# Optimization experiments

Measured on AMD Instinct MI355X. Metric: run time of the kernel, lower is better.

Reference implementation:

```python
import jax, jax.numpy as jnp
import numpy as np

H = 64; W = 64          # input resolution
WS = 8                  # window size
SHIFT = 4               # shift size (= WS//2)
C = 384                 # dim
NH = 12                 # num heads
HD = C // NH            # head dim
HID = 4 * C             # mlp hidden
N = WS * WS             # tokens per window
NWIN = (H // WS) * (W // WS)
EPS = 1e-5


def _rel_pos_index():
    coords = np.stack(np.meshgrid(np.arange(WS), np.arange(WS), indexing='ij'))  # [2,WS,WS]
    flat = coords.reshape(2, -1)                                                 # [2,N]
    rel = flat[:, :, None] - flat[:, None, :]                                    # [2,N,N]
    rel = rel.transpose(1, 2, 0).copy()                                          # [N,N,2]
    rel[..., 0] += WS - 1
    rel[..., 1] += WS - 1
    rel[..., 0] *= 2 * WS - 1
    return rel.sum(-1)                                                           # [N,N]


def _attn_mask():
    img = np.zeros((H, W))
    cnt = 0
    for hs in (slice(0, -WS), slice(-WS, -SHIFT), slice(-SHIFT, None)):
        for ws_ in (slice(0, -WS), slice(-WS, -SHIFT), slice(-SHIFT, None)):
            img[hs, ws_] = cnt
            cnt += 1
    mw = img.reshape(H // WS, WS, W // WS, WS).transpose(0, 2, 1, 3).reshape(-1, N)  # [nW,N]
    diff = mw[:, None, :] - mw[:, :, None]                                           # [nW,N,N]
    return np.where(diff != 0, -100.0, 0.0).astype(np.float32)


_REL_IDX = jnp.asarray(_rel_pos_index())
_MASK = jnp.asarray(_attn_mask())


def _ln(x, g, b):
    m = jnp.mean(x, axis=-1, keepdims=True)
    v = jnp.mean((x - m) ** 2, axis=-1, keepdims=True)
    return (x - m) * jax.lax.rsqrt(v + EPS) * g + b


def _win_partition(x):
    # [B,H,W,C] -> [B*nW, N, C]
    B = x.shape[0]
    x = x.reshape(B, H // WS, WS, W // WS, WS, C).transpose(0, 1, 3, 2, 4, 5)
    return x.reshape(-1, N, C)


def _win_reverse(w, B):
    # [B*nW, N, C] -> [B,H,W,C]
    x = w.reshape(B, H // WS, W // WS, WS, WS, C).transpose(0, 1, 3, 2, 4, 5)
    return x.reshape(B, H, W, C)


def setup_inputs() -> dict:
    key = jax.random.key(0)
    ks = jax.random.split(key, 8)
    s = 0.02
    return {
        'x': jax.random.normal(ks[0], (32, H * W, C), jnp.float32),
        'gamma1': jnp.ones((C,), jnp.float32),
        'beta1': jnp.zeros((C,), jnp.float32),
        'w_qkv': jax.random.normal(ks[1], (C, 3 * C), jnp.float32) * s,
        'b_qkv': jnp.zeros((3 * C,), jnp.float32),
        'bias_table': jax.random.normal(ks[2], ((2 * WS - 1) ** 2, NH), jnp.float32) * s,
        'w_proj': jax.random.normal(ks[3], (C, C), jnp.float32) * s,
        'b_proj': jnp.zeros((C,), jnp.float32),
        'gamma2': jnp.ones((C,), jnp.float32),
        'beta2': jnp.zeros((C,), jnp.float32),
        'w_fc1': jax.random.normal(ks[4], (C, HID), jnp.float32) * s,
        'b_fc1': jnp.zeros((HID,), jnp.float32),
        'w_fc2': jax.random.normal(ks[5], (HID, C), jnp.float32) * s,
        'b_fc2': jnp.zeros((C,), jnp.float32),
    }


def reference(x, gamma1, beta1, w_qkv, b_qkv, bias_table, w_proj, b_proj,
              gamma2, beta2, w_fc1, b_fc1, w_fc2, b_fc2):
    B, L, _ = x.shape
    shortcut = x
    h = _ln(x, gamma1, beta1).reshape(B, H, W, C)
    h = jnp.roll(h, shift=(-SHIFT, -SHIFT), axis=(1, 2))
    xw = _win_partition(h)                                     # [B*nW, N, C]
    Bw = xw.shape[0]

    qkv = (xw @ w_qkv + b_qkv).reshape(Bw, N, 3, NH, HD)
    qkv = qkv.transpose(2, 0, 3, 1, 4)                         # [3, Bw, NH, N, HD]
    q, k, v = qkv[0], qkv[1], qkv[2]
    q = q * (HD ** -0.5)
    attn = jnp.einsum('bhnd,bhmd->bhnm', q, k)                 # [Bw, NH, N, N]

    rel_bias = bias_table[_REL_IDX.reshape(-1)].reshape(N, N, NH).transpose(2, 0, 1)
    attn = attn + rel_bias[None]
    attn = attn.reshape(B, NWIN, NH, N, N) + _MASK[None, :, None]
    attn = jax.nn.softmax(attn.reshape(Bw, NH, N, N), axis=-1)

    out = jnp.einsum('bhnm,bhmd->bhnd', attn, v)               # [Bw, NH, N, HD]
    out = out.transpose(0, 2, 1, 3).reshape(Bw, N, C)
    out = out @ w_proj + b_proj

    h = _win_reverse(out, B)
    h = jnp.roll(h, shift=(SHIFT, SHIFT), axis=(1, 2)).reshape(B, L, C)
    x = shortcut + h

    m = _ln(x, gamma2, beta2)
    m = jax.nn.gelu(m @ w_fc1 + b_fc1, approximate=False) @ w_fc2 + b_fc2
    return x + m
```

## Files before the change

### kernel.cpp

```cpp
#include <hip/hip_runtime.h>
#include <hip/hip_bf16.h>

typedef __bf16 bf16_t;
typedef __bf16 bf16x8 __attribute__((ext_vector_type(8)));
typedef float f32x4 __attribute__((ext_vector_type(4)));

#define DI __device__ __forceinline__

static constexpr int TOK = 131072;
static constexpr int NWIN = 2048;

DI int src_token(int t) {
  int b = t >> 12;
  int widx = (t >> 6) & 63;
  int n = t & 63;
  int wh = widx >> 3, ww = widx & 7;
  int i = n >> 3, j = n & 7;
  int y = ((wh << 3) + i + 4) & 63;
  int x2 = ((ww << 3) + j + 4) & 63;
  return (b << 12) + (y << 6) + x2;
}

DI f32x4 mfma16(bf16x8 a, bf16x8 b, f32x4 c) {
  return __builtin_amdgcn_mfma_f32_16x16x32_bf16(a, b, c, 0, 0, 0);
}

DI void gload_lds16(const bf16_t* g, bf16_t* l) {
  __builtin_amdgcn_global_load_lds(
      (__attribute__((address_space(1))) void*)const_cast<bf16_t*>(g),
      (__attribute__((address_space(3))) void*)l, 16, 0, 0);
}

__global__ void wconv_kernel(const float* __restrict__ w, bf16_t* __restrict__ wt,
                             int K, int N) {
  int idx = blockIdx.x * 256 + threadIdx.x;
  if (idx >= N * K) return;
  int n = idx / K, k = idx - n * K;
  wt[idx] = (bf16_t)w[(size_t)k * N + n];
}

template <int MAP>
__global__ __launch_bounds__(256)
void ln_kernel(const float* __restrict__ xin, const float* __restrict__ g,
               const float* __restrict__ be, bf16_t* __restrict__ out) {
  int w = threadIdx.x >> 6, l = threadIdx.x & 63;
  int t = blockIdx.x * 4 + w;
  int s = MAP ? src_token(t) : t;
  const float* row = xin + (size_t)s * 384;
  float v[6], s1 = 0.f, s2 = 0.f;
#pragma unroll
  for (int i = 0; i < 6; i++) {
    v[i] = row[l + i * 64];
    s1 += v[i];
    s2 += v[i] * v[i];
  }
#pragma unroll
  for (int o = 32; o; o >>= 1) {
    s1 += __shfl_xor(s1, o);
    s2 += __shfl_xor(s2, o);
  }
  float mean = s1 * (1.f / 384.f);
  float var = s2 * (1.f / 384.f) - mean * mean;
  float rs = rsqrtf(var + 1e-5f);
  bf16_t* orow = out + (size_t)t * 384;
#pragma unroll
  for (int i = 0; i < 6; i++) {
    int idx = l + i * 64;
    orow[idx] = (bf16_t)((v[i] - mean) * rs * g[idx] + be[idx]);
  }
}

template <int MODE>
__global__ __launch_bounds__(256, 4)
void gemm_bt(const bf16_t* __restrict__ A, const bf16_t* __restrict__ Wt,
             const float* __restrict__ bias, int K, int ldout, int ncols,
             bf16_t* outb, float* outf, const float* resid) {
  __shared__ __align__(16) bf16_t Alds[128 * 64];
  __shared__ __align__(16) bf16_t Blds[128 * 64];
  const int tid = threadIdx.x;
  const int l = tid & 63, w = tid >> 6;
  const int lr = l & 15, lq = l >> 4;
  const int nwg = gridDim.x;
  const int orig = blockIdx.x;
  const int wgid = (orig & 7) * (nwg >> 3) + (orig >> 3);
  const int bn = wgid % ncols, bm = wgid / ncols;
  const int wr = w >> 1, wc = w & 1;
  const size_t rowA0 = (size_t)bm * 128, rowB0 = (size_t)bn * 128;

  f32x4 acc[4][4] = {};
  for (int k0 = 0; k0 < K; k0 += 64) {
#pragma unroll
    for (int r = 0; r < 4; r++) {
      int offb = r * 2048 + w * 512;
      int off = offb + l * 8;
      int row = off >> 6;
      int slot = (off >> 3) & 7;
      int scol = (slot ^ (row & 7)) << 3;
      gload_lds16(A + (rowA0 + row) * K + k0 + scol, &Alds[offb]);
      gload_lds16(Wt + (rowB0 + row) * K + k0 + scol, &Blds[offb]);
    }
    __syncthreads();
#pragma unroll
    for (int ks = 0; ks < 2; ks++) {
      bf16x8 af[4], bfr[4];
#pragma unroll
      for (int fi = 0; fi < 4; fi++) {
        int row = wr * 64 + fi * 16 + lr;
        af[fi] = *(const bf16x8*)&Alds[row * 64 +
                                       ((ks * 32 + lq * 8) ^ ((row & 7) << 3))];
      }
#pragma unroll
      for (int fj = 0; fj < 4; fj++) {
        int row = wc * 64 + fj * 16 + lr;
        bfr[fj] = *(const bf16x8*)&Blds[row * 64 +
                                        ((ks * 32 + lq * 8) ^ ((row & 7) << 3))];
      }
#pragma unroll
      for (int fi = 0; fi < 4; fi++)
#pragma unroll
        for (int fj = 0; fj < 4; fj++)
          acc[fi][fj] = mfma16(af[fi], bfr[fj], acc[fi][fj]);
    }
    __syncthreads();
  }

#pragma unroll
  for (int fi = 0; fi < 4; fi++) {
#pragma unroll
    for (int reg = 0; reg < 4; reg++) {
      int grow = bm * 128 + wr * 64 + fi * 16 + lq * 4 + reg;
      size_t rbase;
      if constexpr (MODE == 2)
        rbase = (size_t)src_token(grow) * ldout;
      else
        rbase = (size_t)grow * ldout;
#pragma unroll
      for (int fj = 0; fj < 4; fj++) {
        int gcol = bn * 128 + wc * 64 + fj * 16 + lr;
        float val = acc[fi][fj][reg] + bias[gcol];
        if constexpr (MODE == 0) {
          outb[rbase + gcol] = (bf16_t)val;
        } else if constexpr (MODE == 1) {
          val = 0.5f * val * (1.f + erff(val * 0.70710678118f));
          outb[rbase + gcol] = (bf16_t)val;
        } else {
          outf[rbase + gcol] = val + resid[rbase + gcol];
        }
      }
    }
  }
}

__global__ __launch_bounds__(64)
void attn_kernel(const bf16_t* __restrict__ qkv, const float* __restrict__ btab,
                 bf16_t* __restrict__ aout) {
  __shared__ __align__(16) bf16_t Qs[64 * 32];
  __shared__ __align__(16) bf16_t Ks[64 * 32];
  __shared__ __align__(16) bf16_t Vt[32 * 64];
  __shared__ __align__(16) bf16_t Ps[64 * 64];
  const int win = blockIdx.x, h = blockIdx.y;
  const int l = threadIdx.x, lr = l & 15, lq = l >> 4;

  {
    const bf16_t* qrow = qkv + ((size_t)win * 64 + l) * 1152 + h * 32;
#pragma unroll
    for (int c = 0; c < 4; c++) {
      *(bf16x8*)&Qs[l * 32 + c * 8] = *(const bf16x8*)&qrow[c * 8];
      *(bf16x8*)&Ks[l * 32 + c * 8] = *(const bf16x8*)&qrow[384 + c * 8];
    }
#pragma unroll
    for (int c = 0; c < 4; c++) {
      bf16x8 tv = *(const bf16x8*)&qrow[768 + c * 8];
#pragma unroll
      for (int e = 0; e < 8; e++) {
        int vr = c * 8 + e;
        Vt[vr * 64 + (l ^ ((vr & 7) << 3))] = tv[e];
      }
    }
  }
  __syncthreads();

  f32x4 sacc[4][4] = {};
  {
    bf16x8 a[4], b[4];
#pragma unroll
    for (int fi = 0; fi < 4; fi++)
      a[fi] = *(const bf16x8*)&Qs[(fi * 16 + lr) * 32 + lq * 8];
#pragma unroll
    for (int fj = 0; fj < 4; fj++)
      b[fj] = *(const bf16x8*)&Ks[(fj * 16 + lr) * 32 + lq * 8];
#pragma unroll
    for (int fi = 0; fi < 4; fi++)
#pragma unroll
      for (int fj = 0; fj < 4; fj++)
        sacc[fi][fj] = mfma16(a[fi], b[fj], sacc[fi][fj]);
  }

  const int widx = win & 63;
  const int wh = widx >> 3, ww = widx & 7;
  const float scale = 0.17677669529663687f;
#pragma unroll
  for (int fi = 0; fi < 4; fi++) {
#pragma unroll
    for (int reg = 0; reg < 4; reg++) {
      int row = fi * 16 + lq * 4 + reg;
      int i1 = row >> 3, j1 = row & 7;
      int ly1 = (wh == 7) ? (i1 >= 4 ? 2 : 1) : 0;
      int lx1 = (ww == 7) ? (j1 >= 4 ? 2 : 1) : 0;
      float vals[4], m = -1e30f;
#pragma unroll
      for (int fj = 0; fj < 4; fj++) {
        int col = fj * 16 + lr;
        int i2 = col >> 3, j2 = col & 7;
        float v = sacc[fi][fj][reg] * scale +
                  btab[((i1 - i2 + 7) * 15 + (j1 - j2 + 7)) * 12 + h];
        int ly2 = (wh == 7) ? (i2 >= 4 ? 2 : 1) : 0;
        int lx2 = (ww == 7) ? (j2 >= 4 ? 2 : 1) : 0;
        if (ly1 != ly2 || lx1 != lx2) v -= 100.f;
        vals[fj] = v;
        m = fmaxf(m, v);
      }
#pragma unroll
      for (int o = 1; o < 16; o <<= 1) m = fmaxf(m, __shfl_xor(m, o));
      float ssum = 0.f;
#pragma unroll
      for (int fj = 0; fj < 4; fj++) {
        vals[fj] = __expf(vals[fj] - m);
        ssum += vals[fj];
      }
#pragma unroll
      for (int o = 1; o < 16; o <<= 1) ssum += __shfl_xor(ssum, o);
      float inv = 1.f / ssum;
      int sw = (row & 7) << 3;
#pragma unroll
      for (int fj = 0; fj < 4; fj++)
        Ps[row * 64 + ((fj * 16 + lr) ^ sw)] = (bf16_t)(vals[fj] * inv);
    }
  }
  __syncthreads();

  f32x4 oacc[4][2] = {};
#pragma unroll
  for (int kc = 0; kc < 2; kc++) {
    bf16x8 pa[4], vb[2];
#pragma unroll
    for (int fi = 0; fi < 4; fi++) {
      int row = fi * 16 + lr;
      pa[fi] = *(const bf16x8*)&Ps[row * 64 + ((kc * 32 + lq * 8) ^ ((row & 7) << 3))];
    }
#pragma unroll
    for (int fj = 0; fj < 2; fj++) {
      int row = fj * 16 + lr;
      vb[fj] = *(const bf16x8*)&Vt[row * 64 + ((kc * 32 + lq * 8) ^ ((row & 7) << 3))];
    }
#pragma unroll
    for (int fi = 0; fi < 4; fi++)
#pragma unroll
      for (int fj = 0; fj < 2; fj++)
        oacc[fi][fj] = mfma16(pa[fi], vb[fj], oacc[fi][fj]);
  }
#pragma unroll
  for (int fi = 0; fi < 4; fi++)
#pragma unroll
    for (int reg = 0; reg < 4; reg++) {
      int row = fi * 16 + lq * 4 + reg;
      size_t rb = ((size_t)win * 64 + row) * 384 + h * 32;
#pragma unroll
      for (int fj = 0; fj < 2; fj++)
        aout[rb + fj * 16 + lr] = (bf16_t)oacc[fi][fj][reg];
    }
}

extern "C" void kernel_launch(void* const* d_in, const int* in_sizes, int n_in,
                              void* d_out, int out_size, void* d_ws, size_t ws_size,
                              hipStream_t stream) {
  (void)in_sizes; (void)n_in; (void)out_size; (void)ws_size;
  const float* x      = (const float*)d_in[0];
  const float* gamma1 = (const float*)d_in[1];
  const float* beta1  = (const float*)d_in[2];
  const float* w_qkv  = (const float*)d_in[3];
  const float* b_qkv  = (const float*)d_in[4];
  const float* btab   = (const float*)d_in[5];
  const float* w_proj = (const float*)d_in[6];
  const float* b_proj = (const float*)d_in[7];
  const float* gamma2 = (const float*)d_in[8];
  const float* beta2  = (const float*)d_in[9];
  const float* w_fc1  = (const float*)d_in[10];
  const float* b_fc1  = (const float*)d_in[11];
  const float* w_fc2  = (const float*)d_in[12];
  const float* b_fc2  = (const float*)d_in[13];
  float* out = (float*)d_out;

  char* ws = (char*)d_ws;
  size_t off = 0;
  auto alloc = [&](size_t bytes) {
    void* p = ws + off;
    off += (bytes + 255) & ~(size_t)255;
    return p;
  };
  bf16_t* wqkvT  = (bf16_t*)alloc((size_t)1152 * 384 * 2);
  bf16_t* wprojT = (bf16_t*)alloc((size_t)384 * 384 * 2);
  bf16_t* wfc1T  = (bf16_t*)alloc((size_t)1536 * 384 * 2);
  bf16_t* wfc2T  = (bf16_t*)alloc((size_t)384 * 1536 * 2);
  char* big = (char*)alloc((size_t)TOK * 1536 * 2);
  bf16_t* bufA = (bf16_t*)big;
  bf16_t* bufH = (bf16_t*)big;
  bf16_t* bufB = (bf16_t*)alloc((size_t)TOK * 384 * 2);

  wconv_kernel<<<(1152 * 384 + 255) / 256, 256, 0, stream>>>(w_qkv, wqkvT, 384, 1152);
  wconv_kernel<<<(384 * 384 + 255) / 256, 256, 0, stream>>>(w_proj, wprojT, 384, 384);
  wconv_kernel<<<(384 * 1536 + 255) / 256, 256, 0, stream>>>(w_fc1, wfc1T, 384, 1536);
  wconv_kernel<<<(1536 * 384 + 255) / 256, 256, 0, stream>>>(w_fc2, wfc2T, 1536, 384);

  ln_kernel<1><<<TOK / 4, 256, 0, stream>>>(x, gamma1, beta1, bufB);
  gemm_bt<0><<<9 * (TOK / 128), 256, 0, stream>>>(
      bufB, wqkvT, b_qkv, 384, 1152, 9, bufA, nullptr, nullptr);
  attn_kernel<<<dim3(NWIN, 12), 64, 0, stream>>>(bufA, btab, bufB);
  gemm_bt<2><<<3 * (TOK / 128), 256, 0, stream>>>(
      bufB, wprojT, b_proj, 384, 384, 3, nullptr, out, x);
  ln_kernel<0><<<TOK / 4, 256, 0, stream>>>(out, gamma2, beta2, bufB);
  gemm_bt<1><<<12 * (TOK / 128), 256, 0, stream>>>(
      bufB, wfc1T, b_fc1, 384, 1536, 12, bufH, nullptr, nullptr);
  gemm_bt<3><<<3 * (TOK / 128), 256, 0, stream>>>(
      bufH, wfc2T, b_fc2, 1536, 384, 3, nullptr, out, out);
}
```

Measured before the change: 1.212 ms.

## Replace LDS-staged GEMM with direct global-to-register fragment loads and double buffering

The GEMM no longer stages A and W tiles through shared memory with global_load_lds and barriers. Each wave now loads its MFMA fragments straight from global memory into registers, double-buffered across K steps of 32, and the occupancy hint drops from 4 to 3 blocks. This removes LDS traffic and __syncthreads, but the two waves sharing a row or column block now each fetch the same data, and the 16-byte loads per lane are strided by K, which may hurt coalescing and cache efficiency.

Result: slower. 2.246 ms (+85.4%).

```diff
diff --git a/kernel.cpp b/kernel.cpp
--- a/kernel.cpp
+++ b/kernel.cpp
@@ -25,12 +25,6 @@
   return __builtin_amdgcn_mfma_f32_16x16x32_bf16(a, b, c, 0, 0, 0);
 }
 
-DI void gload_lds16(const bf16_t* g, bf16_t* l) {
-  __builtin_amdgcn_global_load_lds(
-      (__attribute__((address_space(1))) void*)const_cast<bf16_t*>(g),
-      (__attribute__((address_space(3))) void*)l, 16, 0, 0);
-}
-
 __global__ void wconv_kernel(const float* __restrict__ w, bf16_t* __restrict__ wt,
                              int K, int N) {
   int idx = blockIdx.x * 256 + threadIdx.x;
@@ -71,12 +65,10 @@
 }
 
 template <int MODE>
-__global__ __launch_bounds__(256, 4)
-void gemm_bt(const bf16_t* __restrict__ A, const bf16_t* __restrict__ Wt,
-             const float* __restrict__ bias, int K, int ldout, int ncols,
-             bf16_t* outb, float* outf, const float* resid) {
-  __shared__ __align__(16) bf16_t Alds[128 * 64];
-  __shared__ __align__(16) bf16_t Blds[128 * 64];
+__global__ __launch_bounds__(256, 3)
+void gemm_gather(const bf16_t* __restrict__ A, const bf16_t* __restrict__ Wt,
+                 const float* __restrict__ bias, int K, int ldout, int ncols,
+                 bf16_t* outb, float* outf, const float* resid) {
   const int tid = threadIdx.x;
   const int l = tid & 63, w = tid >> 6;
   const int lr = l & 15, lq = l >> 4;
@@ -85,50 +77,50 @@
   const int wgid = (orig & 7) * (nwg >> 3) + (orig >> 3);
   const int bn = wgid % ncols, bm = wgid / ncols;
   const int wr = w >> 1, wc = w & 1;
-  const size_t rowA0 = (size_t)bm * 128, rowB0 = (size_t)bn * 128;
+  const size_t row0 = (size_t)bm * 128 + wr * 64;
+  const size_t col0 = (size_t)bn * 128 + wc * 64;
+
+  const bf16_t* pa = A + (row0 + lr) * K + lq * 8;
+  const bf16_t* pb = Wt + (col0 + lr) * K + lq * 8;
+  const size_t fstride = (size_t)16 * K;
 
   f32x4 acc[4][4] = {};
-  for (int k0 = 0; k0 < K; k0 += 64) {
-#pragma unroll
-    for (int r = 0; r < 4; r++) {
-      int offb = r * 2048 + w * 512;
-      int off = offb + l * 8;
-      int row = off >> 6;
-      int slot = (off >> 3) & 7;
-      int scol = (slot ^ (row & 7)) << 3;
-      gload_lds16(A + (rowA0 + row) * K + k0 + scol, &Alds[offb]);
-      gload_lds16(Wt + (rowB0 + row) * K + k0 + scol, &Blds[offb]);
-    }
-    __syncthreads();
-#pragma unroll
-    for (int ks = 0; ks < 2; ks++) {
-      bf16x8 af[4], bfr[4];
-#pragma unroll
-      for (int fi = 0; fi < 4; fi++) {
-        int row = wr * 64 + fi * 16 + lr;
-        af[fi] = *(const bf16x8*)&Alds[row * 64 +
-                                       ((ks * 32 + lq * 8) ^ ((row & 7) << 3))];
-      }
-#pragma unroll
-      for (int fj = 0; fj < 4; fj++) {
-        int row = wc * 64 + fj * 16 + lr;
-        bfr[fj] = *(const bf16x8*)&Blds[row * 64 +
-                                        ((ks * 32 + lq * 8) ^ ((row & 7) << 3))];
-      }
-#pragma unroll
-      for (int fi = 0; fi < 4; fi++)
-#pragma unroll
-        for (int fj = 0; fj < 4; fj++)
-          acc[fi][fj] = mfma16(af[fi], bfr[fj], acc[fi][fj]);
-    }
-    __syncthreads();
-  }
+  bf16x8 a0[4], b0[4], a1[4], b1[4];
+  const int nk = K >> 5;
+
+  auto load = [&](bf16x8 (&fa)[4], bf16x8 (&fb)[4], int s) {
+    const bf16_t* pas = pa + s * 32;
+    const bf16_t* pbs = pb + s * 32;
+#pragma unroll
+    for (int f = 0; f < 4; f++) {
+      fa[f] = *(const bf16x8*)(pas + f * fstride);
+      fb[f] = *(const bf16x8*)(pbs + f * fstride);
+    }
+  };
+  auto step = [&](bf16x8 (&fa)[4], bf16x8 (&fb)[4]) {
+#pragma unroll
+    for (int fi = 0; fi < 4; fi++)
+#pragma unroll
+      for (int fj = 0; fj < 4; fj++)
+        acc[fi][fj] = mfma16(fa[fi], fb[fj], acc[fi][fj]);
+  };
+
+  load(a0, b0, 0);
+  for (int s = 0; s + 2 < nk; s += 2) {
+    load(a1, b1, s + 1);
+    step(a0, b0);
+    load(a0, b0, s + 2);
+    step(a1, b1);
+  }
+  load(a1, b1, nk - 1);
+  step(a0, b0);
+  step(a1, b1);
 
 #pragma unroll
   for (int fi = 0; fi < 4; fi++) {
 #pragma unroll
     for (int reg = 0; reg < 4; reg++) {
-      int grow = bm * 128 + wr * 64 + fi * 16 + lq * 4 + reg;
+      int grow = (int)row0 + fi * 16 + lq * 4 + reg;
       size_t rbase;
       if constexpr (MODE == 2)
         rbase = (size_t)src_token(grow) * ldout;
@@ -136,7 +128,7 @@
         rbase = (size_t)grow * ldout;
 #pragma unroll
       for (int fj = 0; fj < 4; fj++) {
-        int gcol = bn * 128 + wc * 64 + fj * 16 + lr;
+        int gcol = (int)col0 + fj * 16 + lr;
         float val = acc[fi][fj][reg] + bias[gcol];
         if constexpr (MODE == 0) {
           outb[rbase + gcol] = (bf16_t)val;
@@ -313,14 +305,14 @@
   wconv_kernel<<<(1536 * 384 + 255) / 256, 256, 0, stream>>>(w_fc2, wfc2T, 1536, 384);
 
   ln_kernel<1><<<TOK / 4, 256, 0, stream>>>(x, gamma1, beta1, bufB);
-  gemm_bt<0><<<9 * (TOK / 128), 256, 0, stream>>>(
+  gemm_gather<0><<<9 * (TOK / 128), 256, 0, stream>>>(
       bufB, wqkvT, b_qkv, 384, 1152, 9, bufA, nullptr, nullptr);
   attn_kernel<<<dim3(NWIN, 12), 64, 0, stream>>>(bufA, btab, bufB);
-  gemm_bt<2><<<3 * (TOK / 128), 256, 0, stream>>>(
+  gemm_gather<2><<<3 * (TOK / 128), 256, 0, stream>>>(
       bufB, wprojT, b_proj, 384, 384, 3, nullptr, out, x);
   ln_kernel<0><<<TOK / 4, 256, 0, stream>>>(out, gamma2, beta2, bufB);
-  gemm_bt<1><<<12 * (TOK / 128), 256, 0, stream>>>(
+  gemm_gather<1><<<12 * (TOK / 128), 256, 0, stream>>>(
       bufB, wfc1T, b_fc1, 384, 1536, 12, bufH, nullptr, nullptr);
-  gemm_bt<3><<<3 * (TOK / 128), 256, 0, stream>>>(
+  gemm_gather<3><<<3 * (TOK / 128), 256, 0, stream>>>(
       bufH, wfc2T, b_fc2, 1536, 384, 3, nullptr, out, out);
 }
```

## Double-buffer GEMM LDS tiles and switch GELU to tanh approximation

Applied to the files above, without the earlier changes.

The GEMM kernel now uses two LDS buffers, so global-to-LDS loads for the next K tile are issued while the current tile is computed, with one barrier per tile instead of two. LDS fragment offsets and bias values are precomputed outside the loop. The exact erf GELU is replaced by the tanh-form approximation written as x*sigmoid(...), which is cheaper but differs numerically from the approximate=False reference. Doubling LDS use cuts the launch-bounds occupancy hint from 4 to 2 blocks per CU.

Measured after the change: 1.497 ms. 23.6% more time.

```diff
diff --git a/kernel.cpp b/kernel.cpp
--- a/kernel.cpp
+++ b/kernel.cpp
@@ -71,12 +71,12 @@
 }
 
 template <int MODE>
-__global__ __launch_bounds__(256, 4)
+__global__ __launch_bounds__(256, 2)
 void gemm_bt(const bf16_t* __restrict__ A, const bf16_t* __restrict__ Wt,
              const float* __restrict__ bias, int K, int ldout, int ncols,
              bf16_t* outb, float* outf, const float* resid) {
-  __shared__ __align__(16) bf16_t Alds[128 * 64];
-  __shared__ __align__(16) bf16_t Blds[128 * 64];
+  __shared__ __align__(16) bf16_t Alds[2 * 128 * 64];
+  __shared__ __align__(16) bf16_t Blds[2 * 128 * 64];
   const int tid = threadIdx.x;
   const int l = tid & 63, w = tid >> 6;
   const int lr = l & 15, lq = l >> 4;
@@ -85,45 +85,74 @@
   const int wgid = (orig & 7) * (nwg >> 3) + (orig >> 3);
   const int bn = wgid % ncols, bm = wgid / ncols;
   const int wr = w >> 1, wc = w & 1;
-  const size_t rowA0 = (size_t)bm * 128, rowB0 = (size_t)bn * 128;
+
+  const int srow = w * 8 + (l >> 3);
+  const int scol = ((l & 7) ^ (l >> 3)) << 3;
+  const bf16_t* ga = A + ((size_t)bm * 128 + srow) * K + scol;
+  const bf16_t* gb = Wt + ((size_t)bn * 128 + srow) * K + scol;
+  const size_t k32 = (size_t)32 * K;
+
+  int aoff[8], boff[8];
+#pragma unroll
+  for (int fi = 0; fi < 4; fi++) {
+    int ra = wr * 64 + fi * 16 + lr;
+    int rb = wc * 64 + fi * 16 + lr;
+#pragma unroll
+    for (int ks = 0; ks < 2; ks++) {
+      aoff[fi * 2 + ks] = ra * 64 + ((ks * 32 + lq * 8) ^ ((ra & 7) << 3));
+      boff[fi * 2 + ks] = rb * 64 + ((ks * 32 + lq * 8) ^ ((rb & 7) << 3));
+    }
+  }
 
   f32x4 acc[4][4] = {};
-  for (int k0 = 0; k0 < K; k0 += 64) {
+
+  auto stage = [&](int bb) {
 #pragma unroll
     for (int r = 0; r < 4; r++) {
-      int offb = r * 2048 + w * 512;
-      int off = offb + l * 8;
-      int row = off >> 6;
-      int slot = (off >> 3) & 7;
-      int scol = (slot ^ (row & 7)) << 3;
-      gload_lds16(A + (rowA0 + row) * K + k0 + scol, &Alds[offb]);
-      gload_lds16(Wt + (rowB0 + row) * K + k0 + scol, &Blds[offb]);
-    }
-    __syncthreads();
+      gload_lds16(ga + r * k32, &Alds[bb + r * 2048 + w * 512]);
+      gload_lds16(gb + r * k32, &Blds[bb + r * 2048 + w * 512]);
+    }
+    ga += 64;
+    gb += 64;
+  };
+  auto compute = [&](int bb) {
 #pragma unroll
     for (int ks = 0; ks < 2; ks++) {
       bf16x8 af[4], bfr[4];
 #pragma unroll
-      for (int fi = 0; fi < 4; fi++) {
-        int row = wr * 64 + fi * 16 + lr;
-        af[fi] = *(const bf16x8*)&Alds[row * 64 +
-                                       ((ks * 32 + lq * 8) ^ ((row & 7) << 3))];
-      }
-#pragma unroll
-      for (int fj = 0; fj < 4; fj++) {
-        int row = wc * 64 + fj * 16 + lr;
-        bfr[fj] = *(const bf16x8*)&Blds[row * 64 +
-                                        ((ks * 32 + lq * 8) ^ ((row & 7) << 3))];
-      }
+      for (int fi = 0; fi < 4; fi++)
+        af[fi] = *(const bf16x8*)&Alds[bb + aoff[fi * 2 + ks]];
+#pragma unroll
+      for (int fj = 0; fj < 4; fj++)
+        bfr[fj] = *(const bf16x8*)&Blds[bb + boff[fj * 2 + ks]];
 #pragma unroll
       for (int fi = 0; fi < 4; fi++)
 #pragma unroll
         for (int fj = 0; fj < 4; fj++)
           acc[fi][fj] = mfma16(af[fi], bfr[fj], acc[fi][fj]);
     }
+  };
+
+  const int nt = K >> 6;
+  stage(0);
+  __syncthreads();
+  for (int t = 0; t + 2 < nt; t += 2) {
+    stage(8192);
+    compute(0);
     __syncthreads();
-  }
-
+    stage(0);
+    compute(8192);
+    __syncthreads();
+  }
+  stage(8192);
+  compute(0);
+  __syncthreads();
+  compute(8192);
+
+  float bv[4];
+#pragma unroll
+  for (int fj = 0; fj < 4; fj++)
+    bv[fj] = bias[bn * 128 + wc * 64 + fj * 16 + lr];
 #pragma unroll
   for (int fi = 0; fi < 4; fi++) {
 #pragma unroll
@@ -137,11 +166,12 @@
 #pragma unroll
       for (int fj = 0; fj < 4; fj++) {
         int gcol = bn * 128 + wc * 64 + fj * 16 + lr;
-        float val = acc[fi][fj][reg] + bias[gcol];
+        float val = acc[fi][fj][reg] + bv[fj];
         if constexpr (MODE == 0) {
           outb[rbase + gcol] = (bf16_t)val;
         } else if constexpr (MODE == 1) {
-          val = 0.5f * val * (1.f + erff(val * 0.70710678118f));
+          float z = -1.5957691216f * val * fmaf(0.044715f, val * val, 1.0f);
+          val = val / (1.0f + __expf(z));
           outb[rbase + gcol] = (bf16_t)val;
         } else {
           outf[rbase + gcol] = val + resid[rbase + gcol];
```
